# Performance work log

Measured on AMD Instinct MI355X. Metric: run time of the kernel, lower is better.

The kernel has to match this reference:

```python
import jax, jax.numpy as jnp
import numpy as np

B, DX, DZ = 262144, 8, 4

def setup_inputs() -> dict:
    key = jax.random.key(0)
    kx, kz, kp, kh = jax.random.split(key, 4)
    x = jax.random.normal(kx, (B, DX, 1), dtype=jnp.float32)
    z = jax.random.normal(kz, (B, DZ, 1), dtype=jnp.float32)
    # P must be SPD so that S = H P H^T + R is invertible
    A = jax.random.normal(kp, (B, DX, DX), dtype=jnp.float32)
    P = jnp.matmul(A, jnp.swapaxes(A, -1, -2)) / DX + jnp.eye(DX, dtype=jnp.float32)
    H = jax.random.normal(kh, (DZ, DX), dtype=jnp.float32)
    R = jnp.eye(DZ, dtype=jnp.float32)
    return {"x": x, "z": z, "P": P, "H": H, "R": R}

def reference(x, z, P, H, R):
    # Batched Kalman update; per-batch math identical to the torch forward.
    Ix = jnp.eye(DX, dtype=x.dtype)
    y = z - jnp.einsum('zx,bxo->bzo', H, x)                  # innovation [B,DZ,1]
    PHT = jnp.einsum('bxy,zy->bxz', P, H)                    # P H^T      [B,DX,DZ]
    S = jnp.einsum('zx,bxw->bzw', H, PHT) + R                # H P H^T + R [B,DZ,DZ]
    SI = jnp.linalg.inv(S)
    K = jnp.matmul(PHT, SI)                                  # Kalman gain [B,DX,DZ]
    x_new = x + jnp.matmul(K, y)                             # [B,DX,1]
    I_KH = Ix - jnp.einsum('bxz,zy->bxy', K, H)              # [B,DX,DX]
    P_new = (jnp.matmul(jnp.matmul(I_KH, P), jnp.swapaxes(I_KH, -1, -2))
             + jnp.matmul(jnp.einsum('bxz,zw->bxw', K, R), jnp.swapaxes(K, -1, -2)))
    # torch: cat((x.T, P)) -> [1+DX, DX]; batched -> [B, 1+DX, DX]
    return jnp.concatenate((jnp.swapaxes(x_new, -1, -2), P_new), axis=1)
```

## Files before the change

kernel.cpp:

```cpp
#include <hip/hip_runtime.h>

constexpr int B_N = 262144;
constexpr int DX  = 8;
constexpr int DZ  = 4;

__device__ __forceinline__ int swzP(int i) { return i ^ ((i >> 4) & 7); }
__device__ __forceinline__ int swzX(int i) { return i ^ ((i >> 3) & 1); }
__device__ __forceinline__ int swzO(int i) { return i ^ ((i >> 3) & 1); }

__global__ __launch_bounds__(256) void kalman_update(
    const float* __restrict__ x_in,
    const float* __restrict__ z_in,
    const float* __restrict__ P_in,
    const float* __restrict__ H_in,
    const float* __restrict__ R_in,
    float* __restrict__ out)
{
    __shared__ float4 lds[4 * 1152];

    const int wave = threadIdx.x >> 6;
    const int lane = threadIdx.x & 63;
    float4* const slice = lds + wave * 1152;

    const int wbatch = blockIdx.x * 256 + wave * 64;
    const int b      = wbatch + lane;

    {
        const float4* Pg = reinterpret_cast<const float4*>(P_in) + (size_t)wbatch * 16;
#pragma unroll
        for (int k = 0; k < 16; ++k) {
            const int d = 64 * k + lane;
            slice[swzP(d)] = Pg[d];
        }
        const float4* xg = reinterpret_cast<const float4*>(x_in) + (size_t)wbatch * 2;
#pragma unroll
        for (int k = 0; k < 2; ++k) {
            const int d = 64 * k + lane;
            slice[1024 + swzX(d)] = xg[d];
        }
    }

    float y[DZ];
    {
        const float4 a = reinterpret_cast<const float4*>(z_in)[b];
        y[0] = a.x; y[1] = a.y; y[2] = a.z; y[3] = a.w;
    }

    float H[DZ][DX];
#pragma unroll
    for (int i = 0; i < DZ * DX; ++i) H[i / DX][i % DX] = H_in[i];
    float R[DZ][DZ];
#pragma unroll
    for (int i = 0; i < DZ * DZ; ++i) R[i / DZ][i % DZ] = R_in[i];

    float x[DX];
    {
        const float4 a = slice[1024 + swzX(2 * lane + 0)];
        const float4 c = slice[1024 + swzX(2 * lane + 1)];
        x[0] = a.x; x[1] = a.y; x[2] = a.z; x[3] = a.w;
        x[4] = c.x; x[5] = c.y; x[6] = c.z; x[7] = c.w;
    }
    float P[DX][DX];
#pragma unroll
    for (int c16 = 0; c16 < 16; ++c16) {
        const float4 v = slice[swzP(16 * lane + c16)];
        const int r = c16 >> 1, c = (c16 & 1) * 4;
        P[r][c + 0] = v.x; P[r][c + 1] = v.y; P[r][c + 2] = v.z; P[r][c + 3] = v.w;
    }

#pragma unroll
    for (int zi = 0; zi < DZ; ++zi) {
        float acc = 0.f;
#pragma unroll
        for (int k = 0; k < DX; ++k) acc += H[zi][k] * x[k];
        y[zi] -= acc;
    }

    float PHT[DX][DZ];
#pragma unroll
    for (int i = 0; i < DX; ++i)
#pragma unroll
        for (int j = 0; j < DZ; ++j) {
            float acc = 0.f;
#pragma unroll
            for (int k = 0; k < DX; ++k) acc += P[i][k] * H[j][k];
            PHT[i][j] = acc;
        }

    float S[DZ][DZ];
#pragma unroll
    for (int a = 0; a < DZ; ++a)
#pragma unroll
        for (int c = 0; c < DZ; ++c) {
            float acc = R[a][c];
#pragma unroll
            for (int k = 0; k < DX; ++k) acc += H[a][k] * PHT[k][c];
            S[a][c] = acc;
        }

    float SI[DZ][DZ];
    {
        const float A2323 = S[2][2]*S[3][3] - S[2][3]*S[3][2];
        const float A1323 = S[2][1]*S[3][3] - S[2][3]*S[3][1];
        const float A1223 = S[2][1]*S[3][2] - S[2][2]*S[3][1];
        const float A0323 = S[2][0]*S[3][3] - S[2][3]*S[3][0];
        const float A0223 = S[2][0]*S[3][2] - S[2][2]*S[3][0];
        const float A0123 = S[2][0]*S[3][1] - S[2][1]*S[3][0];
        const float A2313 = S[1][2]*S[3][3] - S[1][3]*S[3][2];
        const float A1313 = S[1][1]*S[3][3] - S[1][3]*S[3][1];
        const float A1213 = S[1][1]*S[3][2] - S[1][2]*S[3][1];
        const float A2312 = S[1][2]*S[2][3] - S[1][3]*S[2][2];
        const float A1312 = S[1][1]*S[2][3] - S[1][3]*S[2][1];
        const float A1212 = S[1][1]*S[2][2] - S[1][2]*S[2][1];
        const float A0313 = S[1][0]*S[3][3] - S[1][3]*S[3][0];
        const float A0213 = S[1][0]*S[3][2] - S[1][2]*S[3][0];
        const float A0312 = S[1][0]*S[2][3] - S[1][3]*S[2][0];
        const float A0212 = S[1][0]*S[2][2] - S[1][2]*S[2][0];
        const float A0113 = S[1][0]*S[3][1] - S[1][1]*S[3][0];
        const float A0112 = S[1][0]*S[2][1] - S[1][1]*S[2][0];

        float det = S[0][0] * (S[1][1]*A2323 - S[1][2]*A1323 + S[1][3]*A1223)
                  - S[0][1] * (S[1][0]*A2323 - S[1][2]*A0323 + S[1][3]*A0223)
                  + S[0][2] * (S[1][0]*A1323 - S[1][1]*A0323 + S[1][3]*A0123)
                  - S[0][3] * (S[1][0]*A1223 - S[1][1]*A0223 + S[1][2]*A0123);
        const float id = 1.0f / det;

        SI[0][0] = id *  (S[1][1]*A2323 - S[1][2]*A1323 + S[1][3]*A1223);
        SI[0][1] = id * -(S[0][1]*A2323 - S[0][2]*A1323 + S[0][3]*A1223);
        SI[0][2] = id *  (S[0][1]*A2313 - S[0][2]*A1313 + S[0][3]*A1213);
        SI[0][3] = id * -(S[0][1]*A2312 - S[0][2]*A1312 + S[0][3]*A1212);
        SI[1][0] = id * -(S[1][0]*A2323 - S[1][2]*A0323 + S[1][3]*A0223);
        SI[1][1] = id *  (S[0][0]*A2323 - S[0][2]*A0323 + S[0][3]*A0223);
        SI[1][2] = id * -(S[0][0]*A2313 - S[0][2]*A0313 + S[0][3]*A0213);
        SI[1][3] = id *  (S[0][0]*A2312 - S[0][2]*A0312 + S[0][3]*A0212);
        SI[2][0] = id *  (S[1][0]*A1323 - S[1][1]*A0323 + S[1][3]*A0123);
        SI[2][1] = id * -(S[0][0]*A1323 - S[0][1]*A0323 + S[0][3]*A0123);
        SI[2][2] = id *  (S[0][0]*A1313 - S[0][1]*A0313 + S[0][3]*A0113);
        SI[2][3] = id * -(S[0][0]*A1312 - S[0][1]*A0312 + S[0][3]*A0112);
        SI[3][0] = id * -(S[1][0]*A1223 - S[1][1]*A0223 + S[1][2]*A0123);
        SI[3][1] = id *  (S[0][0]*A1223 - S[0][1]*A0223 + S[0][2]*A0123);
        SI[3][2] = id * -(S[0][0]*A1213 - S[0][1]*A0213 + S[0][2]*A0113);
        SI[3][3] = id *  (S[0][0]*A1212 - S[0][1]*A0212 + S[0][2]*A0112);
    }

    float K[DX][DZ];
#pragma unroll
    for (int i = 0; i < DX; ++i)
#pragma unroll
        for (int j = 0; j < DZ; ++j) {
            float acc = 0.f;
#pragma unroll
            for (int w = 0; w < DZ; ++w) acc += PHT[i][w] * SI[w][j];
            K[i][j] = acc;
        }

    {
        float xn[DX];
#pragma unroll
        for (int i = 0; i < DX; ++i) {
            float acc = x[i];
#pragma unroll
            for (int zi = 0; zi < DZ; ++zi) acc += K[i][zi] * y[zi];
            xn[i] = acc;
        }
        slice[swzO(18 * lane + 0)] = make_float4(xn[0], xn[1], xn[2], xn[3]);
        slice[swzO(18 * lane + 1)] = make_float4(xn[4], xn[5], xn[6], xn[7]);
    }

#pragma unroll
    for (int i = 0; i < DX; ++i)
#pragma unroll
        for (int j = 0; j < DX; ++j) {
            float acc = P[i][j];
#pragma unroll
            for (int zi = 0; zi < DZ; ++zi) acc -= K[i][zi] * PHT[j][zi];
            P[i][j] = acc;
        }

    float E[DX][DZ];
#pragma unroll
    for (int i = 0; i < DX; ++i)
#pragma unroll
        for (int zi = 0; zi < DZ; ++zi) {
            float acc = 0.f;
#pragma unroll
            for (int w = 0; w < DZ; ++w) acc += K[i][w] * R[w][zi];
#pragma unroll
            for (int k = 0; k < DX; ++k) acc -= P[i][k] * H[zi][k];
            E[i][zi] = acc;
        }

#pragma unroll
    for (int i = 0; i < DX; ++i) {
#pragma unroll
        for (int j = 0; j < DX; ++j) {
            float acc = P[i][j];
#pragma unroll
            for (int zi = 0; zi < DZ; ++zi) acc += E[i][zi] * K[j][zi];
            P[i][j] = acc;
        }
        slice[swzO(18 * lane + 2 + 2 * i)]     = make_float4(P[i][0], P[i][1], P[i][2], P[i][3]);
        slice[swzO(18 * lane + 2 + 2 * i + 1)] = make_float4(P[i][4], P[i][5], P[i][6], P[i][7]);
    }

    {
        float4* Og = reinterpret_cast<float4*>(out) + (size_t)wbatch * 18;
#pragma unroll
        for (int k = 0; k < 18; ++k) {
            const int d = 64 * k + lane;
            Og[d] = slice[swzO(d)];
        }
    }
}

extern "C" void kernel_launch(void* const* d_in, const int* in_sizes, int n_in,
                              void* d_out, int out_size, void* d_ws, size_t ws_size,
                              hipStream_t stream) {
    const float* x = (const float*)d_in[0];
    const float* z = (const float*)d_in[1];
    const float* P = (const float*)d_in[2];
    const float* H = (const float*)d_in[3];
    const float* R = (const float*)d_in[4];
    float* out = (float*)d_out;

    dim3 grid(B_N / 256), block(256);
    hipLaunchKernelGGL(kalman_update, grid, block, 0, stream, x, z, P, H, R, out);
}
```

Measured before the change: 145.8 us.

## Halve LDS staging with direct global-to-LDS loads and two-phase staging

P is now loaded straight into LDS with global_load_lds (no VGPR round-trip), pre-swizzled on the global side. The per-wave LDS slice is halved, so P staging and output staging each run in two rounds of 32 lanes, separated by block-wide barriers. x is read directly from global memory per lane, and occupancy is requested with launch_bounds(256,4). The smaller LDS footprint is meant to raise occupancy, at the cost of extra __syncthreads and half-wave idle phases during staging.

```diff
diff --git a/kernel.cpp b/kernel.cpp
--- a/kernel.cpp
+++ b/kernel.cpp
@@ -4,11 +4,15 @@
 constexpr int DX  = 8;
 constexpr int DZ  = 4;
 
-__device__ __forceinline__ int swzP(int i) { return i ^ ((i >> 4) & 7); }
-__device__ __forceinline__ int swzX(int i) { return i ^ ((i >> 3) & 1); }
-__device__ __forceinline__ int swzO(int i) { return i ^ ((i >> 3) & 1); }
-
-__global__ __launch_bounds__(256) void kalman_update(
+typedef __attribute__((address_space(1))) const void GA1;
+typedef __attribute__((address_space(3))) void LA3;
+
+__device__ __forceinline__ void gll16(const void* g, void* l) {
+    __builtin_amdgcn_global_load_lds((GA1*)g, (LA3*)l, 16, 0, 0);
+}
+__device__ __forceinline__ int swz(int i) { return i ^ ((i >> 4) & 7); }
+
+__global__ __launch_bounds__(256, 4) void kalman_update(
     const float* __restrict__ x_in,
     const float* __restrict__ z_in,
     const float* __restrict__ P_in,
@@ -16,34 +20,30 @@
     const float* __restrict__ R_in,
     float* __restrict__ out)
 {
-    __shared__ float4 lds[4 * 1152];
+    __shared__ float4 lds[4 * 576];
 
     const int wave = threadIdx.x >> 6;
     const int lane = threadIdx.x & 63;
-    float4* const slice = lds + wave * 1152;
+    const int m    = lane & 31;
+    float4* const slice = lds + wave * 576;
 
     const int wbatch = blockIdx.x * 256 + wave * 64;
     const int b      = wbatch + lane;
 
+    const float4* Pg = reinterpret_cast<const float4*>(P_in) + (size_t)wbatch * 16;
+
+#pragma unroll
+    for (int k = 0; k < 8; ++k)
+        gll16(&Pg[swz(64 * k + lane)], &slice[64 * k]);
+
+    float x[DX], y[DZ];
     {
-        const float4* Pg = reinterpret_cast<const float4*>(P_in) + (size_t)wbatch * 16;
-#pragma unroll
-        for (int k = 0; k < 16; ++k) {
-            const int d = 64 * k + lane;
-            slice[swzP(d)] = Pg[d];
-        }
-        const float4* xg = reinterpret_cast<const float4*>(x_in) + (size_t)wbatch * 2;
-#pragma unroll
-        for (int k = 0; k < 2; ++k) {
-            const int d = 64 * k + lane;
-            slice[1024 + swzX(d)] = xg[d];
-        }
-    }
-
-    float y[DZ];
-    {
-        const float4 a = reinterpret_cast<const float4*>(z_in)[b];
-        y[0] = a.x; y[1] = a.y; y[2] = a.z; y[3] = a.w;
+        const float4* xp = reinterpret_cast<const float4*>(x_in) + (size_t)b * 2;
+        const float4 a = xp[0], c = xp[1];
+        x[0] = a.x; x[1] = a.y; x[2] = a.z; x[3] = a.w;
+        x[4] = c.x; x[5] = c.y; x[6] = c.z; x[7] = c.w;
+        const float4 zz = reinterpret_cast<const float4*>(z_in)[b];
+        y[0] = zz.x; y[1] = zz.y; y[2] = zz.z; y[3] = zz.w;
     }
 
     float H[DZ][DX];
@@ -53,20 +53,23 @@
 #pragma unroll
     for (int i = 0; i < DZ * DZ; ++i) R[i / DZ][i % DZ] = R_in[i];
 
-    float x[DX];
-    {
-        const float4 a = slice[1024 + swzX(2 * lane + 0)];
-        const float4 c = slice[1024 + swzX(2 * lane + 1)];
-        x[0] = a.x; x[1] = a.y; x[2] = a.z; x[3] = a.w;
-        x[4] = c.x; x[5] = c.y; x[6] = c.z; x[7] = c.w;
-    }
     float P[DX][DX];
-#pragma unroll
-    for (int c16 = 0; c16 < 16; ++c16) {
-        const float4 v = slice[swzP(16 * lane + c16)];
-        const int r = c16 >> 1, c = (c16 & 1) * 4;
-        P[r][c + 0] = v.x; P[r][c + 1] = v.y; P[r][c + 2] = v.z; P[r][c + 3] = v.w;
-    }
+    auto readP = [&]() {
+#pragma unroll
+        for (int j = 0; j < 16; ++j) {
+            const float4 v = slice[swz(16 * m + j)];
+            const int r = j >> 1, c = (j & 1) * 4;
+            P[r][c + 0] = v.x; P[r][c + 1] = v.y; P[r][c + 2] = v.z; P[r][c + 3] = v.w;
+        }
+    };
+
+    __syncthreads();
+    if (lane < 32) readP();
+    __syncthreads();
+
+#pragma unroll
+    for (int k = 0; k < 8; ++k)
+        gll16(&Pg[512 + swz(64 * k + lane)], &slice[64 * k]);
 
 #pragma unroll
     for (int zi = 0; zi < DZ; ++zi) {
@@ -75,6 +78,9 @@
         for (int k = 0; k < DX; ++k) acc += H[zi][k] * x[k];
         y[zi] -= acc;
     }
+
+    __syncthreads();
+    if (lane >= 32) readP();
 
     float PHT[DX][DZ];
 #pragma unroll
@@ -154,17 +160,13 @@
             K[i][j] = acc;
         }
 
-    {
-        float xn[DX];
-#pragma unroll
-        for (int i = 0; i < DX; ++i) {
-            float acc = x[i];
-#pragma unroll
-            for (int zi = 0; zi < DZ; ++zi) acc += K[i][zi] * y[zi];
-            xn[i] = acc;
-        }
-        slice[swzO(18 * lane + 0)] = make_float4(xn[0], xn[1], xn[2], xn[3]);
-        slice[swzO(18 * lane + 1)] = make_float4(xn[4], xn[5], xn[6], xn[7]);
+    float xn[DX];
+#pragma unroll
+    for (int i = 0; i < DX; ++i) {
+        float acc = x[i];
+#pragma unroll
+        for (int zi = 0; zi < DZ; ++zi) acc += K[i][zi] * y[zi];
+        xn[i] = acc;
     }
 
 #pragma unroll
@@ -191,7 +193,7 @@
         }
 
 #pragma unroll
-    for (int i = 0; i < DX; ++i) {
+    for (int i = 0; i < DX; ++i)
 #pragma unroll
         for (int j = 0; j < DX; ++j) {
             float acc = P[i][j];
@@ -199,17 +201,32 @@
             for (int zi = 0; zi < DZ; ++zi) acc += E[i][zi] * K[j][zi];
             P[i][j] = acc;
         }
-        slice[swzO(18 * lane + 2 + 2 * i)]     = make_float4(P[i][0], P[i][1], P[i][2], P[i][3]);
-        slice[swzO(18 * lane + 2 + 2 * i + 1)] = make_float4(P[i][4], P[i][5], P[i][6], P[i][7]);
-    }
-
-    {
-        float4* Og = reinterpret_cast<float4*>(out) + (size_t)wbatch * 18;
-#pragma unroll
-        for (int k = 0; k < 18; ++k) {
-            const int d = 64 * k + lane;
-            Og[d] = slice[swzO(d)];
-        }
+
+    auto writeOut = [&]() {
+        slice[swz(18 * m + 0)] = make_float4(xn[0], xn[1], xn[2], xn[3]);
+        slice[swz(18 * m + 1)] = make_float4(xn[4], xn[5], xn[6], xn[7]);
+#pragma unroll
+        for (int i = 0; i < DX; ++i) {
+            slice[swz(18 * m + 2 + 2 * i)]     = make_float4(P[i][0], P[i][1], P[i][2], P[i][3]);
+            slice[swz(18 * m + 2 + 2 * i + 1)] = make_float4(P[i][4], P[i][5], P[i][6], P[i][7]);
+        }
+    };
+    float4* Og = reinterpret_cast<float4*>(out) + (size_t)wbatch * 18;
+
+    if (lane < 32) writeOut();
+    __syncthreads();
+#pragma unroll
+    for (int k = 0; k < 9; ++k) {
+        const int d = 64 * k + lane;
+        Og[d] = slice[swz(d)];
+    }
+    __syncthreads();
+    if (lane >= 32) writeOut();
+    __syncthreads();
+#pragma unroll
+    for (int k = 0; k < 9; ++k) {
+        const int d = 64 * k + lane;
+        Og[576 + d] = slice[swz(d)];
     }
 }
 
```

After: 168.9 us. +15.8%, slower.
